# Optimization experiments

Hardware: AMD Instinct MI355X
Metric: run time of the kernel (lower is better)

## Reference

```python
import jax, jax.numpy as jnp
import numpy as np

B, L, D_MODEL, N_HEAD = 8, 1024, 1024, 16
D_K = D_MODEL // N_HEAD  # 64


def setup_inputs() -> dict:
    key = jax.random.key(0)
    ks = jax.random.split(key, 10)
    scale = 1.0 / np.sqrt(D_MODEL)
    inp = {
        "q": jax.random.normal(ks[0], (B, L, D_MODEL), jnp.float32),
        "k": jax.random.normal(ks[1], (B, L, D_MODEL), jnp.float32),
        "v": jax.random.normal(ks[2], (B, L, D_MODEL), jnp.float32),
        "mask": jax.random.randint(ks[3], (B, L, L), 0, 2, jnp.int32),
        # per-head projection weights stacked: [H, d_model, d_k]
        "Wq": jax.random.normal(ks[4], (N_HEAD, D_MODEL, D_K), jnp.float32) * scale,
        "Wk": jax.random.normal(ks[5], (N_HEAD, D_MODEL, D_K), jnp.float32) * scale,
        "Wv": jax.random.normal(ks[6], (N_HEAD, D_MODEL, D_K), jnp.float32) * scale,
        # output projection (Dense with bias): [d_model, d_model], [d_model]
        "Wo": jax.random.normal(ks[7], (D_MODEL, D_MODEL), jnp.float32) * scale,
        "bo": jnp.zeros((D_MODEL,), jnp.float32),
    }
    return inp


def reference(q, k, v, mask, Wq, Wk, Wv, Wo, bo):
    d_k = Wq.shape[-1]
    # per-head projections (mode=1 per-head Dense, no bias), vectorized over heads
    qs = jnp.einsum('bld,hdk->bhlk', q, Wq)  # [B,H,Lq,d_k]
    ks = jnp.einsum('bld,hdk->bhlk', k, Wk)  # [B,H,Lk,d_k]
    vs = jnp.einsum('bld,hdk->bhlk', v, Wv)  # [B,H,Lk,d_v]
    # scaled dot-product attention: batch_dot(q,k,axes=[2,2]) / sqrt(d_k)
    scores = jnp.einsum('bhqd,bhkd->bhqk', qs, ks) / jnp.sqrt(jnp.float32(d_k))
    # additive mask: -1e9 * (1 - mask), broadcast over heads
    scores = scores + (-1e9 * (1.0 - mask.astype(jnp.float32)))[:, None, :, :]
    attn = jax.nn.softmax(scores, axis=-1)           # [B,H,Lq,Lk] (dropout inactive at inference)
    head = jnp.einsum('bhqk,bhkd->bhqd', attn, vs)   # [B,H,Lq,d_v]
    b, h, lq, dv = head.shape
    # Concatenate heads along feature axis (head index major, as in mode=1 Concatenate)
    head_cat = head.transpose(0, 2, 1, 3).reshape(b, lq, h * dv)
    outputs = head_cat @ Wo + bo                     # [B,Lq,d_model] (dropout inactive)
    # attn heads also concatenated along last axis in mode=1
    attn_cat = attn.transpose(0, 2, 1, 3).reshape(b, lq, h * attn.shape[-1])
    return outputs, attn_cat
```

## Files before the change

kernel.cpp:

```cpp
#include <hip/hip_runtime.h>

typedef _Float16 f16;
typedef _Float16 f16x8 __attribute__((ext_vector_type(8)));
typedef _Float16 f16x4 __attribute__((ext_vector_type(4)));
typedef _Float16 f16x2 __attribute__((ext_vector_type(2)));
typedef float f32x4 __attribute__((ext_vector_type(4)));

#define GLOAD_LDS16(g, l) \
    __builtin_amdgcn_global_load_lds((const __attribute__((address_space(1))) void*)(g), \
                                     (__attribute__((address_space(3))) void*)(l), 16, 0, 0)

__device__ __forceinline__ f16x2 cvt_pk_f16(float a, float b) {
    return __builtin_bit_cast(f16x2, __builtin_amdgcn_cvt_pkrtz(a, b));
}

#define SC_LOG2E 0.180336880f

__global__ __launch_bounds__(256) void prep_kernel(const float* __restrict__ q,
        const float* __restrict__ k, const float* __restrict__ v,
        const float* __restrict__ Wq, const float* __restrict__ Wk,
        const float* __restrict__ Wv, const float* __restrict__ Wo,
        const int* __restrict__ mask, f16* __restrict__ qh, f16* __restrict__ wt,
        unsigned* __restrict__ bits) {
    const int bid = blockIdx.x;
    if (bid < 12288) {
        const int z = bid >> 12;
        const float* src = (z == 0) ? q : (z == 1) ? k : v;
        const size_t i = ((size_t)(bid & 4095) * 256 + threadIdx.x) * 8;
        float4 a = *(const float4*)&src[i], b2 = *(const float4*)&src[i + 4];
        f16x8 h;
        h[0] = (f16)a.x; h[1] = (f16)a.y; h[2] = (f16)a.z; h[3] = (f16)a.w;
        h[4] = (f16)b2.x; h[5] = (f16)b2.y; h[6] = (f16)b2.z; h[7] = (f16)b2.w;
        *(f16x8*)&qh[(size_t)z * 8388608 + i] = h;
    } else if (bid < 28672) {
        const int t2 = bid - 12288;
        const int z = t2 >> 12;
        const int t = (t2 & 4095) * 256 + threadIdx.x;
        const int n = t >> 10, d = t & 1023;
        float val;
        if (z < 3) {
            const float* W = (z == 0) ? Wq : (z == 1) ? Wk : Wv;
            val = W[((size_t)(n >> 6) * 1024 + d) * 64 + (n & 63)];
        } else {
            val = Wo[(size_t)d * 1024 + n];
        }
        wt[(size_t)z * 1048576 + (size_t)n * 1024 + d] = (f16)val;
    } else {
        const int t = (bid - 28672) * 256 + threadIdx.x;
        const int4* src = (const int4*)mask + (size_t)t * 8;
        unsigned w = 0;
#pragma unroll
        for (int i = 0; i < 8; ++i) {
            int4 vv = src[i];
            w |= (vv.x != 0 ? 1u : 0u) << (i * 4 + 0);
            w |= (vv.y != 0 ? 1u : 0u) << (i * 4 + 1);
            w |= (vv.z != 0 ? 1u : 0u) << (i * 4 + 2);
            w |= (vv.w != 0 ? 1u : 0u) << (i * 4 + 3);
        }
        bits[t] = w;
    }
}

__global__ __launch_bounds__(256) void proj_kernel(const f16* __restrict__ Ah,
        const f16* __restrict__ Wt, f16* __restrict__ Outp) {
    __shared__ __align__(16) f16 As[128][64];
    __shared__ __align__(16) f16 Bs[128][64];
    const int id = blockIdx.x;
    const int z = id >> 9;
    const int id2 = id & 511;
    const int m0 = ((id2 & 7) * 8 + ((id2 >> 3) & 7)) * 128;
    const int n0 = (id2 >> 6) * 128;
    const f16* A = Ah + (size_t)z * 8388608;
    const f16* Bt = Wt + (size_t)z * 1048576;
    f16* Out = Outp + (size_t)z * 8388608;
    const int tid = threadIdx.x, lane = tid & 63;
    const int w = tid >> 6, wr = w >> 1, wc = w & 1;

    f32x4 acc[4][4];
#pragma unroll
    for (int mi = 0; mi < 4; ++mi)
#pragma unroll
        for (int ni = 0; ni < 4; ++ni) acc[mi][ni] = (f32x4){0.f, 0.f, 0.f, 0.f};

    for (int kt = 0; kt < 16; ++kt) {
        const int k0 = kt * 64;
#pragma unroll
        for (int seg = 0; seg < 4; ++seg) {
            const int ch = seg * 256 + tid, r = ch >> 3, c = ch & 7;
            GLOAD_LDS16(&A[(size_t)(m0 + r) * 1024 + k0 + (c ^ (r & 7)) * 8],
                        (char*)&As[0][0] + (seg * 256 + w * 64) * 16);
            GLOAD_LDS16(&Bt[(size_t)(n0 + r) * 1024 + k0 + (c ^ (r & 7)) * 8],
                        (char*)&Bs[0][0] + (seg * 256 + w * 64) * 16);
        }
        __syncthreads();
#pragma unroll
        for (int ks = 0; ks < 2; ++ks) {
            const int slot = ks * 4 + (lane >> 4);
            f16x8 af[4], bf[4];
#pragma unroll
            for (int mi = 0; mi < 4; ++mi) {
                const int row = wr * 64 + mi * 16 + (lane & 15);
                af[mi] = *(const f16x8*)&As[row][(slot ^ (row & 7)) * 8];
            }
#pragma unroll
            for (int ni = 0; ni < 4; ++ni) {
                const int row = wc * 64 + ni * 16 + (lane & 15);
                bf[ni] = *(const f16x8*)&Bs[row][(slot ^ (row & 7)) * 8];
            }
#pragma unroll
            for (int mi = 0; mi < 4; ++mi)
#pragma unroll
                for (int ni = 0; ni < 4; ++ni)
                    acc[mi][ni] = __builtin_amdgcn_mfma_f32_16x16x32_f16(af[mi], bf[ni], acc[mi][ni], 0, 0, 0);
        }
        __syncthreads();
    }

    const float sc = (z == 0) ? SC_LOG2E : 1.0f;
#pragma unroll
    for (int mi = 0; mi < 4; ++mi)
#pragma unroll
        for (int ni = 0; ni < 4; ++ni) {
            const int row0 = m0 + wr * 64 + mi * 16 + ((lane >> 4) << 2);
            const int col = n0 + wc * 64 + ni * 16 + (lane & 15);
            const int h = col >> 6, kk = col & 63;
            const int b = row0 >> 10, l0 = row0 & 1023;
            if (z < 2) {
#pragma unroll
                for (int r = 0; r < 4; ++r)
                    Out[(((size_t)(b * 16 + h) * 1024) + l0 + r) * 64 + kk] = (f16)(acc[mi][ni][r] * sc);
            } else {
                f16x4 hv;
#pragma unroll
                for (int r = 0; r < 4; ++r) hv[r] = (f16)acc[mi][ni][r];
                *(f16x4*)&Out[((size_t)(b * 16 + h) * 64 + kk) * 1024 + l0] = hv;
            }
        }
}

__global__ __launch_bounds__(256) void out_kernel(const f16* __restrict__ A,
        const f16* __restrict__ Bt, float* __restrict__ O, const float* __restrict__ bias) {
    __shared__ __align__(16) f16 As[128][64];
    __shared__ __align__(16) f16 Bs[128][64];
    const int id2 = blockIdx.x;
    const int m0 = ((id2 & 7) * 8 + ((id2 >> 3) & 7)) * 128;
    const int n0 = (id2 >> 6) * 128;
    const int tid = threadIdx.x, lane = tid & 63;
    const int w = tid >> 6, wr = w >> 1, wc = w & 1;

    f32x4 acc[4][4];
#pragma unroll
    for (int mi = 0; mi < 4; ++mi)
#pragma unroll
        for (int ni = 0; ni < 4; ++ni) acc[mi][ni] = (f32x4){0.f, 0.f, 0.f, 0.f};

    for (int kt = 0; kt < 16; ++kt) {
        const int k0 = kt * 64;
#pragma unroll
        for (int seg = 0; seg < 4; ++seg) {
            const int ch = seg * 256 + tid, r = ch >> 3, c = ch & 7;
            GLOAD_LDS16(&A[(size_t)(m0 + r) * 1024 + k0 + (c ^ (r & 7)) * 8],
                        (char*)&As[0][0] + (seg * 256 + w * 64) * 16);
            GLOAD_LDS16(&Bt[(size_t)(n0 + r) * 1024 + k0 + (c ^ (r & 7)) * 8],
                        (char*)&Bs[0][0] + (seg * 256 + w * 64) * 16);
        }
        __syncthreads();
#pragma unroll
        for (int ks = 0; ks < 2; ++ks) {
            const int slot = ks * 4 + (lane >> 4);
            f16x8 af[4], bf[4];
#pragma unroll
            for (int mi = 0; mi < 4; ++mi) {
                const int row = wr * 64 + mi * 16 + (lane & 15);
                af[mi] = *(const f16x8*)&As[row][(slot ^ (row & 7)) * 8];
            }
#pragma unroll
            for (int ni = 0; ni < 4; ++ni) {
                const int row = wc * 64 + ni * 16 + (lane & 15);
                bf[ni] = *(const f16x8*)&Bs[row][(slot ^ (row & 7)) * 8];
            }
#pragma unroll
            for (int mi = 0; mi < 4; ++mi)
#pragma unroll
                for (int ni = 0; ni < 4; ++ni)
                    acc[mi][ni] = __builtin_amdgcn_mfma_f32_16x16x32_f16(af[mi], bf[ni], acc[mi][ni], 0, 0, 0);
        }
        __syncthreads();
    }

#pragma unroll
    for (int mi = 0; mi < 4; ++mi)
#pragma unroll
        for (int ni = 0; ni < 4; ++ni) {
            const int row0 = m0 + wr * 64 + mi * 16 + ((lane >> 4) << 2);
            const int col = n0 + wc * 64 + ni * 16 + (lane & 15);
            const float bb = bias[col];
#pragma unroll
            for (int r = 0; r < 4; ++r)
                __builtin_nontemporal_store(acc[mi][ni][r] + bb, &O[(size_t)(row0 + r) * 1024 + col]);
        }
}

__global__ __launch_bounds__(256) void attn_fused_kernel(const f16* __restrict__ Qp,
        const f16* __restrict__ Kp, const f16* __restrict__ VpT,
        const unsigned* __restrict__ bits, float* __restrict__ attn, f16* __restrict__ headcat) {
    __shared__ __align__(16) f16 Qs[128][64];
    __shared__ __align__(16) f16 Ks[2][64][64];
    __shared__ __align__(16) f16 Vs[64][64];
    __shared__ __align__(16) f16 Ps[128][64];
    __shared__ unsigned bm[128][32];
    __shared__ __align__(16) float LUTf[16][4];
    __shared__ __align__(16) f16 LUTh[16][4];
    const int bh = blockIdx.x & 127, m0 = (blockIdx.x >> 7) * 128;
    const int b = bh >> 4, h = bh & 15;
    const int tid = threadIdx.x, lane = tid & 63, w = tid >> 6;
    const f16* Qbase = Qp + (size_t)bh * 65536;
    const f16* Kbase = Kp + (size_t)bh * 65536;
    const f16* Vbase = VpT + (size_t)bh * 65536;

    auto stageK = [&](int buf, int j) {
#pragma unroll
        for (int seg = 0; seg < 2; ++seg) {
            const int ch = seg * 256 + tid, r = ch >> 3, c = ch & 7;
            GLOAD_LDS16(&Kbase[(size_t)(j * 64 + r) * 64 + (c ^ (r & 7)) * 8],
                        (char*)&Ks[buf][0][0] + (seg * 256 + w * 64) * 16);
        }
    };
    auto stageV = [&](int j) {
#pragma unroll
        for (int seg = 0; seg < 2; ++seg) {
            const int ch = seg * 256 + tid, r = ch >> 3, c = ch & 7;
            GLOAD_LDS16(&Vbase[(size_t)r * 1024 + j * 64 + (c ^ (r & 7)) * 8],
                        (char*)&Vs[0][0] + (seg * 256 + w * 64) * 16);
        }
    };

    if (tid < 16) {
#pragma unroll
        for (int i = 0; i < 4; ++i) {
            const float on = ((tid >> i) & 1) ? 1.0f : 0.0f;
            LUTf[tid][i] = on;
            LUTh[tid][i] = (f16)on;
        }
    }
#pragma unroll
    for (int seg = 0; seg < 4; ++seg) {
        const int ch = seg * 256 + tid, r = ch >> 3, c = ch & 7;
        GLOAD_LDS16(&Qbase[(size_t)(m0 + r) * 64 + (c ^ (r & 7)) * 8],
                    (char*)&Qs[0][0] + (seg * 256 + w * 64) * 16);
        GLOAD_LDS16((const char*)&bits[((size_t)b * 1024 + m0 + r) * 32] + (c ^ (r & 7)) * 16,
                    (char*)&bm[0][0] + (seg * 256 + w * 64) * 16);
    }
    stageK(0, 0);
    __syncthreads();

    float lsum[2] = {0.f, 0.f};
    const int kb0 = (lane >> 4) * 4;

    for (int j = 0; j < 16; ++j) {
        if (j < 15) stageK((j + 1) & 1, j + 1);

        f32x4 acc[2][4];
#pragma unroll
        for (int mi = 0; mi < 2; ++mi)
#pragma unroll
            for (int ni = 0; ni < 4; ++ni) acc[mi][ni] = (f32x4){0.f, 0.f, 0.f, 0.f};
#pragma unroll
        for (int ks = 0; ks < 2; ++ks) {
            const int slot = ks * 4 + (lane >> 4);
            f16x8 af[2], bf[4];
#pragma unroll
            for (int mi = 0; mi < 2; ++mi) {
                const int row = w * 32 + mi * 16 + (lane & 15);
                af[mi] = *(const f16x8*)&Qs[row][(slot ^ (row & 7)) * 8];
            }
#pragma unroll
            for (int ni = 0; ni < 4; ++ni) {
                const int row = ni * 16 + (lane & 15);
                bf[ni] = *(const f16x8*)&Ks[j & 1][row][(slot ^ (row & 7)) * 8];
            }
#pragma unroll
            for (int mi = 0; mi < 2; ++mi)
#pragma unroll
                for (int ni = 0; ni < 4; ++ni)
                    acc[mi][ni] = __builtin_amdgcn_mfma_f32_16x16x32_f16(bf[ni], af[mi], acc[mi][ni], 0, 0, 0);
        }

#pragma unroll
        for (int mi = 0; mi < 2; ++mi) {
            const int rowm = w * 32 + mi * 16 + (lane & 15);
            const int swb = (rowm & 7) << 2;
#pragma unroll
            for (int ni = 0; ni < 4; ++ni) {
                const unsigned word = bm[rowm][(2 * j + (ni >> 1)) ^ swb];
                const unsigned nib = (word >> (((ni & 1) << 4) + kb0)) & 15u;
                const float4 mf = *(const float4*)&LUTf[nib][0];
                lsum[mi] = fmaf(exp2f(acc[mi][ni][0]), mf.x, lsum[mi]);
                lsum[mi] = fmaf(exp2f(acc[mi][ni][1]), mf.y, lsum[mi]);
                lsum[mi] = fmaf(exp2f(acc[mi][ni][2]), mf.z, lsum[mi]);
                lsum[mi] = fmaf(exp2f(acc[mi][ni][3]), mf.w, lsum[mi]);
            }
        }
        __syncthreads();
    }

    stageK(0, 0);

    f16x2 rlp[2];
#pragma unroll
    for (int mi = 0; mi < 2; ++mi) {
        float s = lsum[mi];
        s += __shfl_xor(s, 16);
        s += __shfl_xor(s, 32);
        const f16 rlh = (f16)(1.0f / s);
        rlp[mi][0] = rlh; rlp[mi][1] = rlh;
    }

    f32x4 accP[2][4];
#pragma unroll
    for (int mi = 0; mi < 2; ++mi)
#pragma unroll
        for (int ni = 0; ni < 4; ++ni) accP[mi][ni] = (f32x4){0.f, 0.f, 0.f, 0.f};

    float* attnBase = attn + ((size_t)b * 1024 + m0) * 16384 + h * 1024;
    const int st_r0 = tid >> 4;
    const int st_c4 = tid & 15;
    __syncthreads();

    for (int j = 0; j < 16; ++j) {
        if (j < 15) stageK((j + 1) & 1, j + 1);
        stageV(j);

        f32x4 acc[2][4];
#pragma unroll
        for (int mi = 0; mi < 2; ++mi)
#pragma unroll
            for (int ni = 0; ni < 4; ++ni) acc[mi][ni] = (f32x4){0.f, 0.f, 0.f, 0.f};
#pragma unroll
        for (int ks = 0; ks < 2; ++ks) {
            const int slot = ks * 4 + (lane >> 4);
            f16x8 af[2], bf[4];
#pragma unroll
            for (int mi = 0; mi < 2; ++mi) {
                const int row = w * 32 + mi * 16 + (lane & 15);
                af[mi] = *(const f16x8*)&Qs[row][(slot ^ (row & 7)) * 8];
            }
#pragma unroll
            for (int ni = 0; ni < 4; ++ni) {
                const int row = ni * 16 + (lane & 15);
                bf[ni] = *(const f16x8*)&Ks[j & 1][row][(slot ^ (row & 7)) * 8];
            }
#pragma unroll
            for (int mi = 0; mi < 2; ++mi)
#pragma unroll
                for (int ni = 0; ni < 4; ++ni)
                    acc[mi][ni] = __builtin_amdgcn_mfma_f32_16x16x32_f16(bf[ni], af[mi], acc[mi][ni], 0, 0, 0);
        }

#pragma unroll
        for (int mi = 0; mi < 2; ++mi) {
            const int rowm = w * 32 + mi * 16 + (lane & 15);
            const int swb = (rowm & 7) << 2;
            const int swp = (rowm & 7) << 3;
#pragma unroll
            for (int ni = 0; ni < 4; ++ni) {
                const unsigned word = bm[rowm][(2 * j + (ni >> 1)) ^ swb];
                const unsigned nib = (word >> (((ni & 1) << 4) + kb0)) & 15u;
                const f16x4 mh = *(const f16x4*)&LUTh[nib][0];
                f16x2 p01 = cvt_pk_f16(exp2f(acc[mi][ni][0]), exp2f(acc[mi][ni][1]));
                f16x2 p23 = cvt_pk_f16(exp2f(acc[mi][ni][2]), exp2f(acc[mi][ni][3]));
                p01 = p01 * (f16x2){mh[0], mh[1]} * rlp[mi];
                p23 = p23 * (f16x2){mh[2], mh[3]} * rlp[mi];
                f16x4 pw; pw[0] = p01[0]; pw[1] = p01[1]; pw[2] = p23[0]; pw[3] = p23[1];
                *(f16x4*)&Ps[rowm][(ni * 16 + kb0) ^ swp] = pw;
            }
        }
        __syncthreads();

#pragma unroll
        for (int ks = 0; ks < 2; ++ks) {
            const int slot = ks * 4 + (lane >> 4);
            f16x8 pf[2], vf[4];
#pragma unroll
            for (int mi = 0; mi < 2; ++mi) {
                const int row = w * 32 + mi * 16 + (lane & 15);
                pf[mi] = *(const f16x8*)&Ps[row][(slot ^ (row & 7)) * 8];
            }
#pragma unroll
            for (int ni = 0; ni < 4; ++ni) {
                const int row = ni * 16 + (lane & 15);
                vf[ni] = *(const f16x8*)&Vs[row][(slot ^ (row & 7)) * 8];
            }
#pragma unroll
            for (int mi = 0; mi < 2; ++mi)
#pragma unroll
                for (int ni = 0; ni < 4; ++ni)
                    accP[mi][ni] = __builtin_amdgcn_mfma_f32_16x16x32_f16(pf[mi], vf[ni], accP[mi][ni], 0, 0, 0);
        }

#pragma unroll
        for (int i = 0; i < 8; ++i) {
            const int row = st_r0 + 16 * i;
            const f16x4 hv = *(const f16x4*)((const char*)&Ps[row][0] +
                    ((st_c4 >> 1) ^ (row & 7)) * 16 + (st_c4 & 1) * 8);
            f32x4 fv = {(float)hv[0], (float)hv[1], (float)hv[2], (float)hv[3]};
            __builtin_nontemporal_store(fv,
                    (f32x4*)&attnBase[(size_t)row * 16384 + j * 64 + st_c4 * 4]);
        }
        __syncthreads();
    }

#pragma unroll
    for (int mi = 0; mi < 2; ++mi)
#pragma unroll
        for (int ni = 0; ni < 4; ++ni) {
            const int row0 = m0 + w * 32 + mi * 16 + ((lane >> 4) << 2);
            const int col = ni * 16 + (lane & 15);
#pragma unroll
            for (int r = 0; r < 4; ++r)
                headcat[((size_t)b * 1024 + row0 + r) * 1024 + h * 64 + col] = (f16)accP[mi][ni][r];
        }
}

extern "C" void kernel_launch(void* const* d_in, const int* in_sizes, int n_in,
                              void* d_out, int out_size, void* d_ws, size_t ws_size,
                              hipStream_t stream) {
    const float* q = (const float*)d_in[0];
    const float* k = (const float*)d_in[1];
    const float* v = (const float*)d_in[2];
    const int* mask = (const int*)d_in[3];
    const float* Wq = (const float*)d_in[4];
    const float* Wk = (const float*)d_in[5];
    const float* Wv = (const float*)d_in[6];
    const float* Wo = (const float*)d_in[7];
    const float* bo = (const float*)d_in[8];

    float* out0 = (float*)d_out;
    float* attn = out0 + (size_t)8 * 1024 * 1024;

    char* ws = (char*)d_ws;
    f16* wt   = (f16*)(ws + ((size_t)0 << 20));
    f16* qh   = (f16*)(ws + ((size_t)8 << 20));
    f16* Qp   = (f16*)(ws + ((size_t)56 << 20));
    f16* Kp   = (f16*)(ws + ((size_t)72 << 20));
    f16* VpT  = (f16*)(ws + ((size_t)88 << 20));
    f16* hc   = (f16*)(ws + ((size_t)104 << 20));
    unsigned* bits = (unsigned*)(ws + ((size_t)120 << 20));
    f16* wot  = wt + (size_t)3 * 1048576;

    prep_kernel<<<29696, 256, 0, stream>>>(q, k, v, Wq, Wk, Wv, Wo, mask, qh, wt, bits);

    proj_kernel<<<1536, 256, 0, stream>>>(qh, wt, Qp);

    attn_fused_kernel<<<1024, 256, 0, stream>>>(Qp, Kp, VpT, bits, attn, hc);

    out_kernel<<<512, 256, 0, stream>>>(hc, wot, out0, bo);
}
```

Measured before the change: 293.0 us.

## Use 512-thread blocks with 16 query rows per wave in attention kernel

Doubles the attention kernel's block to 8 waves, each owning 16 query rows instead of 32. Staging loads are redistributed so each thread issues fewer global-to-LDS copies, and the softmax row sum is split into two accumulators to shorten the dependency chain. The aim is more waves in flight and less register pressure per wave to hide latency. In exchange, each wave reloads the K and V fragments for half as many rows, and barriers now synchronise more waves.

```diff
diff --git a/kernel.cpp b/kernel.cpp
--- a/kernel.cpp
+++ b/kernel.cpp
@@ -201,7 +201,7 @@
         }
 }
 
-__global__ __launch_bounds__(256) void attn_fused_kernel(const f16* __restrict__ Qp,
+__global__ __launch_bounds__(512, 4) void attn_fused_kernel(const f16* __restrict__ Qp,
         const f16* __restrict__ Kp, const f16* __restrict__ VpT,
         const unsigned* __restrict__ bits, float* __restrict__ attn, f16* __restrict__ headcat) {
     __shared__ __align__(16) f16 Qs[128][64];
@@ -214,25 +214,20 @@
     const int bh = blockIdx.x & 127, m0 = (blockIdx.x >> 7) * 128;
     const int b = bh >> 4, h = bh & 15;
     const int tid = threadIdx.x, lane = tid & 63, w = tid >> 6;
+    const int l15 = lane & 15, t4 = lane >> 4;
     const f16* Qbase = Qp + (size_t)bh * 65536;
     const f16* Kbase = Kp + (size_t)bh * 65536;
     const f16* Vbase = VpT + (size_t)bh * 65536;
 
     auto stageK = [&](int buf, int j) {
-#pragma unroll
-        for (int seg = 0; seg < 2; ++seg) {
-            const int ch = seg * 256 + tid, r = ch >> 3, c = ch & 7;
-            GLOAD_LDS16(&Kbase[(size_t)(j * 64 + r) * 64 + (c ^ (r & 7)) * 8],
-                        (char*)&Ks[buf][0][0] + (seg * 256 + w * 64) * 16);
-        }
+        const int r = tid >> 3, c = tid & 7;
+        GLOAD_LDS16(&Kbase[(size_t)(j * 64 + r) * 64 + (c ^ (r & 7)) * 8],
+                    (char*)&Ks[buf][0][0] + (size_t)tid * 16);
     };
     auto stageV = [&](int j) {
-#pragma unroll
-        for (int seg = 0; seg < 2; ++seg) {
-            const int ch = seg * 256 + tid, r = ch >> 3, c = ch & 7;
-            GLOAD_LDS16(&Vbase[(size_t)r * 1024 + j * 64 + (c ^ (r & 7)) * 8],
-                        (char*)&Vs[0][0] + (seg * 256 + w * 64) * 16);
-        }
+        const int r = tid >> 3, c = tid & 7;
+        GLOAD_LDS16(&Vbase[(size_t)r * 1024 + j * 64 + (c ^ (r & 7)) * 8],
+                    (char*)&Vs[0][0] + (size_t)tid * 16);
     };
 
     if (tid < 16) {
@@ -244,83 +239,67 @@
         }
     }
 #pragma unroll
-    for (int seg = 0; seg < 4; ++seg) {
-        const int ch = seg * 256 + tid, r = ch >> 3, c = ch & 7;
+    for (int seg = 0; seg < 2; ++seg) {
+        const int ch = seg * 512 + tid, r = ch >> 3, c = ch & 7;
         GLOAD_LDS16(&Qbase[(size_t)(m0 + r) * 64 + (c ^ (r & 7)) * 8],
-                    (char*)&Qs[0][0] + (seg * 256 + w * 64) * 16);
+                    (char*)&Qs[0][0] + (size_t)ch * 16);
         GLOAD_LDS16((const char*)&bits[((size_t)b * 1024 + m0 + r) * 32] + (c ^ (r & 7)) * 16,
-                    (char*)&bm[0][0] + (seg * 256 + w * 64) * 16);
+                    (char*)&bm[0][0] + (size_t)ch * 16);
     }
     stageK(0, 0);
     __syncthreads();
 
-    float lsum[2] = {0.f, 0.f};
-    const int kb0 = (lane >> 4) * 4;
+    const int rowm = w * 16 + l15;
+    const int swb = (rowm & 7) << 2;
+    const int swp = (rowm & 7) << 3;
+    const int kb0 = t4 * 4;
+    float lsA = 0.f, lsB = 0.f;
 
     for (int j = 0; j < 16; ++j) {
         if (j < 15) stageK((j + 1) & 1, j + 1);
 
-        f32x4 acc[2][4];
-#pragma unroll
-        for (int mi = 0; mi < 2; ++mi)
-#pragma unroll
-            for (int ni = 0; ni < 4; ++ni) acc[mi][ni] = (f32x4){0.f, 0.f, 0.f, 0.f};
+        f32x4 acc[4];
+#pragma unroll
+        for (int ni = 0; ni < 4; ++ni) acc[ni] = (f32x4){0.f, 0.f, 0.f, 0.f};
 #pragma unroll
         for (int ks = 0; ks < 2; ++ks) {
-            const int slot = ks * 4 + (lane >> 4);
-            f16x8 af[2], bf[4];
-#pragma unroll
-            for (int mi = 0; mi < 2; ++mi) {
-                const int row = w * 32 + mi * 16 + (lane & 15);
-                af[mi] = *(const f16x8*)&Qs[row][(slot ^ (row & 7)) * 8];
-            }
+            const int slot = ks * 4 + t4;
+            const f16x8 af = *(const f16x8*)&Qs[rowm][(slot ^ (rowm & 7)) * 8];
 #pragma unroll
             for (int ni = 0; ni < 4; ++ni) {
-                const int row = ni * 16 + (lane & 15);
-                bf[ni] = *(const f16x8*)&Ks[j & 1][row][(slot ^ (row & 7)) * 8];
-            }
-#pragma unroll
-            for (int mi = 0; mi < 2; ++mi)
-#pragma unroll
-                for (int ni = 0; ni < 4; ++ni)
-                    acc[mi][ni] = __builtin_amdgcn_mfma_f32_16x16x32_f16(bf[ni], af[mi], acc[mi][ni], 0, 0, 0);
-        }
-
-#pragma unroll
-        for (int mi = 0; mi < 2; ++mi) {
-            const int rowm = w * 32 + mi * 16 + (lane & 15);
-            const int swb = (rowm & 7) << 2;
-#pragma unroll
-            for (int ni = 0; ni < 4; ++ni) {
-                const unsigned word = bm[rowm][(2 * j + (ni >> 1)) ^ swb];
-                const unsigned nib = (word >> (((ni & 1) << 4) + kb0)) & 15u;
-                const float4 mf = *(const float4*)&LUTf[nib][0];
-                lsum[mi] = fmaf(exp2f(acc[mi][ni][0]), mf.x, lsum[mi]);
-                lsum[mi] = fmaf(exp2f(acc[mi][ni][1]), mf.y, lsum[mi]);
-                lsum[mi] = fmaf(exp2f(acc[mi][ni][2]), mf.z, lsum[mi]);
-                lsum[mi] = fmaf(exp2f(acc[mi][ni][3]), mf.w, lsum[mi]);
-            }
+                const int row = ni * 16 + l15;
+                const f16x8 bf = *(const f16x8*)&Ks[j & 1][row][(slot ^ (row & 7)) * 8];
+                acc[ni] = __builtin_amdgcn_mfma_f32_16x16x32_f16(bf, af, acc[ni], 0, 0, 0);
+            }
+        }
+
+#pragma unroll
+        for (int ni = 0; ni < 4; ++ni) {
+            const unsigned word = bm[rowm][(2 * j + (ni >> 1)) ^ swb];
+            const unsigned nib = (word >> (((ni & 1) << 4) + kb0)) & 15u;
+            const float4 mf = *(const float4*)&LUTf[nib][0];
+            lsA = fmaf(exp2f(acc[ni][0]), mf.x, lsA);
+            lsB = fmaf(exp2f(acc[ni][1]), mf.y, lsB);
+            lsA = fmaf(exp2f(acc[ni][2]), mf.z, lsA);
+            lsB = fmaf(exp2f(acc[ni][3]), mf.w, lsB);
         }
         __syncthreads();
     }
 
     stageK(0, 0);
 
-    f16x2 rlp[2];
-#pragma unroll
-    for (int mi = 0; mi < 2; ++mi) {
-        float s = lsum[mi];
+    f16x2 rlp;
+    {
+        float s = lsA + lsB;
         s += __shfl_xor(s, 16);
         s += __shfl_xor(s, 32);
         const f16 rlh = (f16)(1.0f / s);
-        rlp[mi][0] = rlh; rlp[mi][1] = rlh;
-    }
-
-    f32x4 accP[2][4];
-#pragma unroll
-    for (int mi = 0; mi < 2; ++mi)
-#pragma unroll
-        for (int ni = 0; ni < 4; ++ni) accP[mi][ni] = (f32x4){0.f, 0.f, 0.f, 0.f};
+        rlp[0] = rlh; rlp[1] = rlh;
+    }
+
+    f32x4 accP[4];
+#pragma unroll
+    for (int ni = 0; ni < 4; ++ni) accP[ni] = (f32x4){0.f, 0.f, 0.f, 0.f};
 
     float* attnBase = attn + ((size_t)b * 1024 + m0) * 16384 + h * 1024;
     const int st_r0 = tid >> 4;
@@ -331,76 +310,50 @@
         if (j < 15) stageK((j + 1) & 1, j + 1);
         stageV(j);
 
-        f32x4 acc[2][4];
-#pragma unroll
-        for (int mi = 0; mi < 2; ++mi)
-#pragma unroll
-            for (int ni = 0; ni < 4; ++ni) acc[mi][ni] = (f32x4){0.f, 0.f, 0.f, 0.f};
+        f32x4 acc[4];
+#pragma unroll
+        for (int ni = 0; ni < 4; ++ni) acc[ni] = (f32x4){0.f, 0.f, 0.f, 0.f};
 #pragma unroll
         for (int ks = 0; ks < 2; ++ks) {
-            const int slot = ks * 4 + (lane >> 4);
-            f16x8 af[2], bf[4];
-#pragma unroll
-            for (int mi = 0; mi < 2; ++mi) {
-                const int row = w * 32 + mi * 16 + (lane & 15);
-                af[mi] = *(const f16x8*)&Qs[row][(slot ^ (row & 7)) * 8];
-            }
+            const int slot = ks * 4 + t4;
+            const f16x8 af = *(const f16x8*)&Qs[rowm][(slot ^ (rowm & 7)) * 8];
 #pragma unroll
             for (int ni = 0; ni < 4; ++ni) {
-                const int row = ni * 16 + (lane & 15);
-                bf[ni] = *(const f16x8*)&Ks[j & 1][row][(slot ^ (row & 7)) * 8];
-            }
-#pragma unroll
-            for (int mi = 0; mi < 2; ++mi)
-#pragma unroll
-                for (int ni = 0; ni < 4; ++ni)
-                    acc[mi][ni] = __builtin_amdgcn_mfma_f32_16x16x32_f16(bf[ni], af[mi], acc[mi][ni], 0, 0, 0);
-        }
-
-#pragma unroll
-        for (int mi = 0; mi < 2; ++mi) {
-            const int rowm = w * 32 + mi * 16 + (lane & 15);
-            const int swb = (rowm & 7) << 2;
-            const int swp = (rowm & 7) << 3;
+                const int row = ni * 16 + l15;
+                const f16x8 bf = *(const f16x8*)&Ks[j & 1][row][(slot ^ (row & 7)) * 8];
+                acc[ni] = __builtin_amdgcn_mfma_f32_16x16x32_f16(bf, af, acc[ni], 0, 0, 0);
+            }
+        }
+
+#pragma unroll
+        for (int ni = 0; ni < 4; ++ni) {
+            const unsigned word = bm[rowm][(2 * j + (ni >> 1)) ^ swb];
+            const unsigned nib = (word >> (((ni & 1) << 4) + kb0)) & 15u;
+            const f16x4 mh = *(const f16x4*)&LUTh[nib][0];
+            f16x2 p01 = cvt_pk_f16(exp2f(acc[ni][0]), exp2f(acc[ni][1]));
+            f16x2 p23 = cvt_pk_f16(exp2f(acc[ni][2]), exp2f(acc[ni][3]));
+            p01 = p01 * (f16x2){mh[0], mh[1]} * rlp;
+            p23 = p23 * (f16x2){mh[2], mh[3]} * rlp;
+            f16x4 pw; pw[0] = p01[0]; pw[1] = p01[1]; pw[2] = p23[0]; pw[3] = p23[1];
+            *(f16x4*)&Ps[rowm][(ni * 16 + kb0) ^ swp] = pw;
+        }
+        __syncthreads();
+
+#pragma unroll
+        for (int ks = 0; ks < 2; ++ks) {
+            const int slot = ks * 4 + t4;
+            const f16x8 pf = *(const f16x8*)&Ps[rowm][(slot ^ (rowm & 7)) * 8];
 #pragma unroll
             for (int ni = 0; ni < 4; ++ni) {
-                const unsigned word = bm[rowm][(2 * j + (ni >> 1)) ^ swb];
-                const unsigned nib = (word >> (((ni & 1) << 4) + kb0)) & 15u;
-                const f16x4 mh = *(const f16x4*)&LUTh[nib][0];
-                f16x2 p01 = cvt_pk_f16(exp2f(acc[mi][ni][0]), exp2f(acc[mi][ni][1]));
-                f16x2 p23 = cvt_pk_f16(exp2f(acc[mi][ni][2]), exp2f(acc[mi][ni][3]));
-                p01 = p01 * (f16x2){mh[0], mh[1]} * rlp[mi];
-                p23 = p23 * (f16x2){mh[2], mh[3]} * rlp[mi];
-                f16x4 pw; pw[0] = p01[0]; pw[1] = p01[1]; pw[2] = p23[0]; pw[3] = p23[1];
-                *(f16x4*)&Ps[rowm][(ni * 16 + kb0) ^ swp] = pw;
-            }
-        }
-        __syncthreads();
-
-#pragma unroll
-        for (int ks = 0; ks < 2; ++ks) {
-            const int slot = ks * 4 + (lane >> 4);
-            f16x8 pf[2], vf[4];
-#pragma unroll
-            for (int mi = 0; mi < 2; ++mi) {
-                const int row = w * 32 + mi * 16 + (lane & 15);
-                pf[mi] = *(const f16x8*)&Ps[row][(slot ^ (row & 7)) * 8];
-            }
-#pragma unroll
-            for (int ni = 0; ni < 4; ++ni) {
-                const int row = ni * 16 + (lane & 15);
-                vf[ni] = *(const f16x8*)&Vs[row][(slot ^ (row & 7)) * 8];
-            }
-#pragma unroll
-            for (int mi = 0; mi < 2; ++mi)
-#pragma unroll
-                for (int ni = 0; ni < 4; ++ni)
-                    accP[mi][ni] = __builtin_amdgcn_mfma_f32_16x16x32_f16(pf[mi], vf[ni], accP[mi][ni], 0, 0, 0);
-        }
-
-#pragma unroll
-        for (int i = 0; i < 8; ++i) {
-            const int row = st_r0 + 16 * i;
+                const int row = ni * 16 + l15;
+                const f16x8 vf = *(const f16x8*)&Vs[row][(slot ^ (row & 7)) * 8];
+                accP[ni] = __builtin_amdgcn_mfma_f32_16x16x32_f16(pf, vf, accP[ni], 0, 0, 0);
+            }
+        }
+
+#pragma unroll
+        for (int i = 0; i < 4; ++i) {
+            const int row = st_r0 + 32 * i;
             const f16x4 hv = *(const f16x4*)((const char*)&Ps[row][0] +
                     ((st_c4 >> 1) ^ (row & 7)) * 16 + (st_c4 & 1) * 8);
             f32x4 fv = {(float)hv[0], (float)hv[1], (float)hv[2], (float)hv[3]};
@@ -411,15 +364,13 @@
     }
 
 #pragma unroll
-    for (int mi = 0; mi < 2; ++mi)
-#pragma unroll
-        for (int ni = 0; ni < 4; ++ni) {
-            const int row0 = m0 + w * 32 + mi * 16 + ((lane >> 4) << 2);
-            const int col = ni * 16 + (lane & 15);
-#pragma unroll
-            for (int r = 0; r < 4; ++r)
-                headcat[((size_t)b * 1024 + row0 + r) * 1024 + h * 64 + col] = (f16)accP[mi][ni][r];
-        }
+    for (int ni = 0; ni < 4; ++ni) {
+        const int row0 = m0 + w * 16 + (t4 << 2);
+        const int col = ni * 16 + l15;
+#pragma unroll
+        for (int r = 0; r < 4; ++r)
+            headcat[((size_t)b * 1024 + row0 + r) * 1024 + h * 64 + col] = (f16)accP[ni][r];
+    }
 }
 
 extern "C" void kernel_launch(void* const* d_in, const int* in_sizes, int n_in,
@@ -452,7 +403,7 @@
 
     proj_kernel<<<1536, 256, 0, stream>>>(qh, wt, Qp);
 
-    attn_fused_kernel<<<1024, 256, 0, stream>>>(Qp, Kp, VpT, bits, attn, hc);
+    attn_fused_kernel<<<1024, 512, 0, stream>>>(Qp, Kp, VpT, bits, attn, hc);
 
     out_kernel<<<512, 256, 0, stream>>>(hc, wot, out0, bo);
 }
```

Measured after the change: 283.9 us. 3.1% less time.
